# Kernel tuning notes

Hardware: AMD Instinct MI355X
Metric: run time of the kernel (lower is better)

The kernel has to match this reference:

```python
import jax, jax.numpy as jnp
import numpy as np

# ---- HashGridPlanesEncoder config (hybrid-k-planes) ----
NUM_LEVELS = 16
LEVEL_DIM = 2
BASE_RES = 16
DESIRED_RES = 2048
LOG2_HASHMAP = 19
D = 2  # grid_nd: each plane encoder is a 2D hash grid
N_PTS = 1048576
COO_COMBS = [(0, 1), (0, 2), (1, 2)]
HASH_PRIME_1 = 2654435761  # torch-ngp fast_hash prime for dim 1 (dim 0 prime is 1)


def _level_constants():
    # Mirrors torch-ngp GridEncoder offset/resolution computation.
    pls = 2.0 ** (np.log2(DESIRED_RES / BASE_RES) / (NUM_LEVELS - 1))
    max_params = 2 ** LOG2_HASHMAP
    scales, res, sizes, offs = [], [], [], [0]
    for l in range(NUM_LEVELS):
        s = BASE_RES * pls ** l - 1.0          # kernel: scale = exp2(l*S + H) - 1
        r = int(np.ceil(s)) + 1                # kernel: resolution = ceil(scale) + 1
        p = min(max_params, (r + 1) ** D)      # align_corners=False -> (res+1)^D
        p = int(np.ceil(p / 8) * 8)            # round up to multiple of 8
        scales.append(s); res.append(r); sizes.append(p); offs.append(offs[-1] + p)
    return (np.array(scales, np.float32), np.array(res, np.int64),
            np.array(sizes, np.int64), np.array(offs[:-1], np.int64), offs[-1])


SCALES, RES, SIZES, OFFSETS, TOTAL_PARAMS = _level_constants()
USE_HASH = ((RES + 1) ** D) > SIZES  # static per-level: dense linear index vs spatial hash


def _encode_plane(x2, table):
    """x2: [N,2] coords in [0,1]; table: [TOTAL_PARAMS, LEVEL_DIM]. Returns [N, L*C]."""
    n = x2.shape[0]
    scales = jnp.asarray(SCALES)
    pos = x2[:, None, :] * scales[None, :, None] + 0.5           # [N,L,2] (align_corners=False)
    pg_f = jnp.floor(pos)
    frac = pos - pg_f                                            # [N,L,2]
    pg = pg_f.astype(jnp.uint32)
    corners = jnp.array([[0, 0], [1, 0], [0, 1], [1, 1]], jnp.uint32)  # [4,2]
    cpos = pg[:, :, None, :] + corners[None, None]               # [N,L,4,2]
    cmask = corners.astype(bool)[None, None]                     # [1,1,4,2]
    w = jnp.where(cmask, frac[:, :, None, :], 1.0 - frac[:, :, None, :]).prod(-1)  # [N,L,4]
    stride1 = jnp.asarray((RES + 1).astype(np.uint32))           # [L]
    linear = cpos[..., 0] + cpos[..., 1] * stride1[None, :, None]
    hashed = cpos[..., 0] ^ (cpos[..., 1] * jnp.uint32(HASH_PRIME_1))  # uint32 wrap-around
    idx = jnp.where(jnp.asarray(USE_HASH)[None, :, None], hashed, linear)
    idx = idx % jnp.asarray(SIZES.astype(np.uint32))[None, :, None]
    idx = (idx + jnp.asarray(OFFSETS.astype(np.uint32))[None, :, None]).astype(jnp.int32)
    feats = table[idx]                                           # [N,L,4,C] gather
    out = (w[..., None] * feats).sum(axis=2)                     # [N,L,C] bilinear interp
    return out.reshape(n, NUM_LEVELS * LEVEL_DIM)


def setup_inputs() -> dict:
    key = jax.random.key(0)
    kp, k0, k1, k2 = jax.random.split(key, 4)
    pts = jax.random.uniform(kp, (N_PTS, 3), dtype=jnp.float32)  # coords (treated as in [-1,1] domain)
    std = 1e-4  # GridEncoder init: embeddings.uniform_(-1e-4, 1e-4)
    mk = lambda k: jax.random.uniform(k, (TOTAL_PARAMS, LEVEL_DIM), jnp.float32, -std, std)
    return {"pts": pts, "table_xy": mk(k0), "table_xz": mk(k1), "table_yz": mk(k2)}


def reference(pts, table_xy, table_xz, table_yz):
    # GridEncoder.forward normalizes inputs: (x + bound) / (2*bound), bound=1
    u = (pts + 1.0) * 0.5
    tables = (table_xy, table_xz, table_yz)
    out = _encode_plane(u[:, list(COO_COMBS[0])], tables[0])
    for comb, tab in zip(COO_COMBS[1:], tables[1:]):
        out = out + _encode_plane(u[:, list(comb)], tab)
    return out
```

## Files before the change

### kernel.cpp

```cpp
#include <hip/hip_runtime.h>
#include <hip/hip_fp16.h>
#include <cmath>

#define NLEV 16
#define HASH_START 12
#define HMASK ((1u << 19) - 1u)
#define HASH_PRIME 2654435761u
#define LDS_WORDS 14160

typedef float    f4 __attribute__((ext_vector_type(4)));
typedef unsigned u4 __attribute__((ext_vector_type(4)));

struct LvlC {
  float scale[NLEV];
  unsigned stride[NLEV];
  unsigned offset[NLEV];
};

__device__ __forceinline__ float2 h2f(unsigned u) {
  return __half22float2(__builtin_bit_cast(__half2, u));
}

__global__ __launch_bounds__(256) void k_convert(
    const float2* __restrict__ t0, const float2* __restrict__ t1,
    const float2* __restrict__ t2, unsigned* __restrict__ dst, unsigned total)
{
  unsigned g = blockIdx.x * 256 + threadIdx.x;
  unsigned stp = gridDim.x * 256;
  unsigned tot3 = 3u * total;
  for (unsigned e = g; e < tot3; e += stp) {
    const float2* src; unsigned i = e;
    if (i < total)            { src = t0; }
    else if (i < 2u * total)  { src = t1; i -= total; }
    else                      { src = t2; i -= 2u * total; }
    float2 v = src[i];
    __half2 h = __floats2half2_rn(v.x, v.y);
    __builtin_nontemporal_store(__builtin_bit_cast(unsigned, h), dst + e);
  }
}

__global__ __launch_bounds__(256) void k_dense(
    const float* __restrict__ pts, const unsigned* __restrict__ tab,
    unsigned* __restrict__ slices,
    LvlC lc, unsigned total, int n)
{
  int i = blockIdx.x * 256 + threadIdx.x;
  if (i >= n) return;
  float u0 = (pts[3 * i + 0] + 1.f) * .5f;
  float u1 = (pts[3 * i + 1] + 1.f) * .5f;
  float u2 = (pts[3 * i + 2] + 1.f) * .5f;
  const float ua[3] = {u0, u0, u1}, ub[3] = {u1, u2, u2};

#pragma unroll 1
  for (int grp = 0; grp < 3; ++grp) {
    const int l0 = 6 + 2 * grp;
    uint2 g[2][3][2];
    float gx[2][3], gy[2][3];
#pragma unroll
    for (int h = 0; h < 2; ++h) {
      const float sc = lc.scale[l0 + h];
      const unsigned st = lc.stride[l0 + h], o = lc.offset[l0 + h];
#pragma unroll
      for (int p = 0; p < 3; ++p) {
        float px = ua[p] * sc + .5f, py = ub[p] * sc + .5f;
        float fx = floorf(px), fy = floorf(py);
        gx[h][p] = px - fx; gy[h][p] = py - fy;
        unsigned i00 = (unsigned)fx + (unsigned)fy * st + o;
        const unsigned* tp = tab + (size_t)p * total;
        g[h][p][0] = *reinterpret_cast<const uint2*>(tp + i00);
        g[h][p][1] = *reinterpret_cast<const uint2*>(tp + i00 + st);
      }
    }
#pragma unroll
    for (int h = 0; h < 2; ++h) {
      float s0 = 0.f, s1 = 0.f;
#pragma unroll
      for (int p = 0; p < 3; ++p) {
        float x = gx[h][p], y = gy[h][p];
        float w00 = (1.f - x) * (1.f - y), w10 = x * (1.f - y);
        float w01 = (1.f - x) * y,          w11 = x * y;
        float2 f00 = h2f(g[h][p][0].x), f10 = h2f(g[h][p][0].y);
        float2 f01 = h2f(g[h][p][1].x), f11 = h2f(g[h][p][1].y);
        s0 += w00 * f00.x + w10 * f10.x + w01 * f01.x + w11 * f11.x;
        s1 += w00 * f00.y + w10 * f10.y + w01 * f01.y + w11 * f11.y;
      }
      __builtin_nontemporal_store(
          __builtin_bit_cast(unsigned, __floats2half2_rn(s0, s1)),
          slices + (size_t)(2 * grp + h) * n + i);
    }
  }
}

__device__ __forceinline__ void hash_row(
    const unsigned* __restrict__ tp, unsigned x0, unsigned hy,
    unsigned& g0, unsigned& g1)
{
  unsigned a0 = (x0 ^ hy) & HMASK;
  if ((x0 & 1u) == 0u) {
    uint2 v = *reinterpret_cast<const uint2*>(tp + (a0 & ~1u));
    bool hi = (a0 & 1u) != 0u;
    g0 = hi ? v.y : v.x;
    g1 = hi ? v.x : v.y;
  } else {
    g0 = tp[a0];
    g1 = tp[((x0 + 1u) ^ hy) & HMASK];
  }
}

__global__ __launch_bounds__(256) void k_hash(
    const float* __restrict__ pts, const unsigned* __restrict__ tab,
    unsigned* __restrict__ slices,
    LvlC lc, unsigned total, int n)
{
  int i = blockIdx.x * 256 + threadIdx.x;
  if (i >= n) return;
  float u0 = (pts[3 * i + 0] + 1.f) * .5f;
  float u1 = (pts[3 * i + 1] + 1.f) * .5f;
  float u2 = (pts[3 * i + 2] + 1.f) * .5f;
  const float ua[3] = {u0, u0, u1}, ub[3] = {u1, u2, u2};

#pragma unroll 1
  for (int grp = 0; grp < 2; ++grp) {
    const int l0 = HASH_START + 2 * grp;
    unsigned g[2][3][4];
    float rx[2][3], ry[2][3];
#pragma unroll
    for (int h = 0; h < 2; ++h) {
      const float sc = lc.scale[l0 + h];
      const unsigned o = lc.offset[l0 + h];
#pragma unroll
      for (int p = 0; p < 3; ++p) {
        float px = ua[p] * sc + .5f, py = ub[p] * sc + .5f;
        float fx = floorf(px), fy = floorf(py);
        rx[h][p] = px - fx; ry[h][p] = py - fy;
        unsigned x0 = (unsigned)fx, y0 = (unsigned)fy;
        unsigned hy0 = y0 * HASH_PRIME, hy1 = hy0 + HASH_PRIME;
        const unsigned* tp = tab + (size_t)p * total + o;
        hash_row(tp, x0, hy0, g[h][p][0], g[h][p][1]);
        hash_row(tp, x0, hy1, g[h][p][2], g[h][p][3]);
      }
    }
#pragma unroll
    for (int h = 0; h < 2; ++h) {
      float s0 = 0.f, s1 = 0.f;
#pragma unroll
      for (int p = 0; p < 3; ++p) {
        float x = rx[h][p], y = ry[h][p];
        float w00 = (1.f - x) * (1.f - y), w10 = x * (1.f - y);
        float w01 = (1.f - x) * y,          w11 = x * y;
        float2 f00 = h2f(g[h][p][0]), f10 = h2f(g[h][p][1]);
        float2 f01 = h2f(g[h][p][2]), f11 = h2f(g[h][p][3]);
        s0 += w00 * f00.x + w10 * f10.x + w01 * f01.x + w11 * f11.x;
        s1 += w00 * f00.y + w10 * f10.y + w01 * f01.y + w11 * f11.y;
      }
      __builtin_nontemporal_store(
          __builtin_bit_cast(unsigned, __floats2half2_rn(s0, s1)),
          slices + (size_t)(2 * grp + h) * n + i);
    }
  }
}

__global__ __launch_bounds__(512) void k_final(
    const float* __restrict__ pts, const unsigned* __restrict__ tab,
    const unsigned* __restrict__ slices,
    float* __restrict__ out, LvlC lc, unsigned total, int n)
{
  __shared__ unsigned lds[LDS_WORDS];
  int half = n >> 1;
  int t = blockIdx.x * 512 + threadIdx.x;
  const int idx[2] = {t, t + half};

  unsigned sl[2][10];
#pragma unroll
  for (int k = 0; k < 2; ++k)
#pragma unroll
    for (int j = 0; j < 10; ++j) sl[k][j] = slices[(size_t)j * n + idx[k]];

  float ua[2][3], ub[2][3];
#pragma unroll
  for (int k = 0; k < 2; ++k) {
    float u0 = (pts[3 * idx[k] + 0] + 1.f) * .5f;
    float u1 = (pts[3 * idx[k] + 1] + 1.f) * .5f;
    float u2 = (pts[3 * idx[k] + 2] + 1.f) * .5f;
    ua[k][0] = u0; ub[k][0] = u1;
    ua[k][1] = u0; ub[k][1] = u2;
    ua[k][2] = u1; ub[k][2] = u2;
  }

  float res[2][12];
#pragma unroll
  for (int k = 0; k < 2; ++k)
#pragma unroll
    for (int j = 0; j < 12; ++j) res[k][j] = 0.f;

  for (int p = 0; p < 3; ++p) {
    if (p) __syncthreads();
    const u4* src = reinterpret_cast<const u4*>(tab + (size_t)p * total);
    for (unsigned e = threadIdx.x; e < LDS_WORDS / 4; e += 512)
      reinterpret_cast<u4*>(lds)[e] = src[e];
    __syncthreads();
#pragma unroll
    for (int l = 0; l < 6; ++l) {
      const float sc = lc.scale[l];
      const unsigned st = lc.stride[l], o = lc.offset[l];
#pragma unroll
      for (int k = 0; k < 2; ++k) {
        float px = ua[k][p] * sc + .5f, py = ub[k][p] * sc + .5f;
        float fx = floorf(px), fy = floorf(py);
        float x = px - fx, y = py - fy;
        unsigned i00 = (unsigned)fx + (unsigned)fy * st + o;
        float2 f00 = h2f(lds[i00]),      f10 = h2f(lds[i00 + 1]);
        float2 f01 = h2f(lds[i00 + st]), f11 = h2f(lds[i00 + st + 1]);
        float w00 = (1.f - x) * (1.f - y), w10 = x * (1.f - y);
        float w01 = (1.f - x) * y,          w11 = x * y;
        res[k][2 * l + 0] += w00 * f00.x + w10 * f10.x + w01 * f01.x + w11 * f11.x;
        res[k][2 * l + 1] += w00 * f00.y + w10 * f10.y + w01 * f01.y + w11 * f11.y;
      }
    }
  }

#pragma unroll
  for (int k = 0; k < 2; ++k) {
    float v[32];
#pragma unroll
    for (int j = 0; j < 12; ++j) v[j] = res[k][j];
#pragma unroll
    for (int j = 0; j < 10; ++j) {
      float2 f = h2f(sl[k][j]);
      v[12 + 2 * j] = f.x; v[12 + 2 * j + 1] = f.y;
    }
    float4* o4 = (float4*)(out + (size_t)idx[k] * 32);
#pragma unroll
    for (int j = 0; j < 8; ++j)
      o4[j] = make_float4(v[4 * j], v[4 * j + 1], v[4 * j + 2], v[4 * j + 3]);
  }
}

__global__ __launch_bounds__(256) void k_fallback(
    const float* __restrict__ pts, const float2* __restrict__ txy,
    const float2* __restrict__ txz, const float2* __restrict__ tyz,
    float* __restrict__ out, LvlC lc, int n)
{
  int i = blockIdx.x * 256 + threadIdx.x;
  if (i >= n) return;
  float u0 = (pts[3 * i + 0] + 1.f) * .5f;
  float u1 = (pts[3 * i + 1] + 1.f) * .5f;
  float u2 = (pts[3 * i + 2] + 1.f) * .5f;
  const float ua[3] = {u0, u0, u1}, ub[3] = {u1, u2, u2};
  const float2* tabs[3] = {txy, txz, tyz};
  float acc[32];
#pragma unroll
  for (int j = 0; j < 32; ++j) acc[j] = 0.f;
#pragma unroll
  for (int l = 0; l < NLEV; ++l) {
    const float sc = lc.scale[l];
    const unsigned o = lc.offset[l], s = lc.stride[l];
#pragma unroll
    for (int p = 0; p < 3; ++p) {
      const float2* t = tabs[p];
      float px = ua[p] * sc + .5f, py = ub[p] * sc + .5f;
      float fx = floorf(px), fy = floorf(py);
      float rx = px - fx, ry = py - fy;
      unsigned x0 = (unsigned)fx, y0 = (unsigned)fy;
      float w00 = (1.f - rx) * (1.f - ry), w10 = rx * (1.f - ry);
      float w01 = (1.f - rx) * ry,          w11 = rx * ry;
      float2 f00, f10, f01, f11;
      if (l >= HASH_START) {
        unsigned hy0 = y0 * HASH_PRIME, hy1 = hy0 + HASH_PRIME;
        f00 = t[o + ((x0 ^ hy0) & HMASK)];
        f10 = t[o + (((x0 + 1u) ^ hy0) & HMASK)];
        f01 = t[o + ((x0 ^ hy1) & HMASK)];
        f11 = t[o + (((x0 + 1u) ^ hy1) & HMASK)];
      } else {
        unsigned i00 = x0 + y0 * s;
        float4 r0 = *reinterpret_cast<const float4*>(t + o + i00);
        float4 r1 = *reinterpret_cast<const float4*>(t + o + i00 + s);
        f00 = make_float2(r0.x, r0.y); f10 = make_float2(r0.z, r0.w);
        f01 = make_float2(r1.x, r1.y); f11 = make_float2(r1.z, r1.w);
      }
      acc[2 * l + 0] += w00 * f00.x + w10 * f10.x + w01 * f01.x + w11 * f11.x;
      acc[2 * l + 1] += w00 * f00.y + w10 * f10.y + w01 * f01.y + w11 * f11.y;
    }
  }
  float4* o4 = (float4*)(out + (size_t)i * 32);
#pragma unroll
  for (int j = 0; j < 8; ++j)
    o4[j] = make_float4(acc[4 * j], acc[4 * j + 1], acc[4 * j + 2], acc[4 * j + 3]);
}

static unsigned compute_levels(LvlC* lc)
{
  const double pls = std::pow(2.0, std::log2(2048.0 / 16.0) / 15.0);
  unsigned long long off = 0;
  for (int l = 0; l < NLEV; ++l) {
    double s = 16.0 * std::pow(pls, (double)l) - 1.0;
    lc->scale[l] = (float)s;
    long long r = (long long)std::ceil(s) + 1;
    long long dense = (r + 1) * (r + 1);
    long long sz = dense < (1LL << 19) ? dense : (1LL << 19);
    sz = ((sz + 7) / 8) * 8;
    lc->stride[l] = (unsigned)(r + 1);
    lc->offset[l] = (unsigned)off;
    off += (unsigned long long)sz;
  }
  return (unsigned)off;
}

extern "C" void kernel_launch(void* const* d_in, const int* in_sizes, int n_in,
                              void* d_out, int out_size, void* d_ws, size_t ws_size,
                              hipStream_t stream) {
  const float*  pts = (const float*)d_in[0];
  const float2* txy = (const float2*)d_in[1];
  const float2* txz = (const float2*)d_in[2];
  const float2* tyz = (const float2*)d_in[3];
  float* out = (float*)d_out;
  int n = in_sizes[0] / 3;

  LvlC lc;
  unsigned total = compute_levels(&lc);

  size_t tab_bytes = (size_t)3 * total * 4;
  size_t tab_al = (tab_bytes + 255) & ~(size_t)255;
  size_t need = tab_al + (size_t)10 * n * 4;

  bool ok = (n % 1024 == 0) && (lc.offset[6] == LDS_WORDS) && (ws_size >= need);
  for (int l = HASH_START; l < NLEV; ++l) {
    unsigned sz = ((l + 1 < NLEV) ? lc.offset[l + 1] : total) - lc.offset[l];
    ok = ok && (sz == (1u << 19));
  }

  int block = 256;
  int grid = (n + block - 1) / block;
  if (!ok) {
    k_fallback<<<grid, block, 0, stream>>>(pts, txy, txz, tyz, out, lc, n);
    return;
  }

  unsigned* tab16 = (unsigned*)d_ws;
  unsigned* slices = (unsigned*)((char*)d_ws + tab_al);

  k_convert<<<2048, 256, 0, stream>>>(txy, txz, tyz, tab16, total);
  k_dense<<<grid, block, 0, stream>>>(pts, tab16, slices, lc, total, n);
  k_hash <<<grid, block, 0, stream>>>(pts, tab16, slices + (size_t)6 * n, lc, total, n);
  k_final<<<(n / 2) / 512, 512, 0, stream>>>(pts, tab16, slices, out, lc, total, n);
}
```

Baseline: 382.1 us.

## Duplicate dense rows into interleaved fp16 layout, gather hash levels from fp32 directly

Replaces the full-table fp16 conversion with a small conversion of levels 0-5 plus a row-duplicated layout for dense levels 6-11, so each bilinear lookup becomes a single 16-byte load. Hash levels now read the original fp32 tables directly, which removes the need to convert the large hash tables at all. The dense and hash kernels are merged into one gather kernel. The final kernel now handles four points per thread in a 2048-point block so the LDS table load is amortised better. The cost is more launches for the duplication step, wider fp32 hash loads, and more register pressure in the final kernel.

```diff
diff --git a/kernel.cpp b/kernel.cpp
--- a/kernel.cpp
+++ b/kernel.cpp
@@ -15,34 +15,66 @@
   float scale[NLEV];
   unsigned stride[NLEV];
   unsigned offset[NLEV];
+  unsigned dupoff[NLEV];
 };
 
 __device__ __forceinline__ float2 h2f(unsigned u) {
   return __half22float2(__builtin_bit_cast(__half2, u));
 }
 
-__global__ __launch_bounds__(256) void k_convert(
+__global__ __launch_bounds__(256) void k_convert05(
     const float2* __restrict__ t0, const float2* __restrict__ t1,
-    const float2* __restrict__ t2, unsigned* __restrict__ dst, unsigned total)
-{
-  unsigned g = blockIdx.x * 256 + threadIdx.x;
-  unsigned stp = gridDim.x * 256;
-  unsigned tot3 = 3u * total;
-  for (unsigned e = g; e < tot3; e += stp) {
-    const float2* src; unsigned i = e;
-    if (i < total)            { src = t0; }
-    else if (i < 2u * total)  { src = t1; i -= total; }
-    else                      { src = t2; i -= 2u * total; }
-    float2 v = src[i];
-    __half2 h = __floats2half2_rn(v.x, v.y);
-    __builtin_nontemporal_store(__builtin_bit_cast(unsigned, h), dst + e);
-  }
-}
-
-__global__ __launch_bounds__(256) void k_dense(
-    const float* __restrict__ pts, const unsigned* __restrict__ tab,
-    unsigned* __restrict__ slices,
-    LvlC lc, unsigned total, int n)
+    const float2* __restrict__ t2, unsigned* __restrict__ dst, unsigned total16)
+{
+  unsigned idx = blockIdx.x * 256 + threadIdx.x;
+  if (idx >= 3u * LDS_WORDS) return;
+  unsigned p = idx / LDS_WORDS, e = idx % LDS_WORDS;
+  const float2* src = (p == 0) ? t0 : ((p == 1) ? t1 : t2);
+  float2 v = src[e];
+  dst[(size_t)p * total16 + e] =
+      __builtin_bit_cast(unsigned, __floats2half2_rn(v.x, v.y));
+}
+
+__global__ __launch_bounds__(256) void k_convert_dup(
+    const float2* __restrict__ t0, const float2* __restrict__ t1,
+    const float2* __restrict__ t2, unsigned* __restrict__ dst,
+    unsigned src_off, unsigned dst_off, unsigned st, unsigned total16)
+{
+  unsigned x = blockIdx.x * 256 + threadIdx.x;
+  if (x >= st) return;
+  unsigned y = blockIdx.y;
+  unsigned p = blockIdx.z;
+  const float2* src = (p == 0) ? t0 : ((p == 1) ? t1 : t2);
+  float2 a = src[src_off + (size_t)y * st + x];
+  float2 b = src[src_off + (size_t)(y + 1) * st + x];
+  uint2 w;
+  w.x = __builtin_bit_cast(unsigned, __floats2half2_rn(a.x, a.y));
+  w.y = __builtin_bit_cast(unsigned, __floats2half2_rn(b.x, b.y));
+  *reinterpret_cast<uint2*>(dst + (size_t)p * total16 + dst_off +
+                            (size_t)(y * st + x) * 2) = w;
+}
+
+__device__ __forceinline__ void hash_row_f32(
+    const float2* __restrict__ tp, unsigned x0, unsigned hy,
+    float2& g0, float2& g1)
+{
+  unsigned a0 = (x0 ^ hy) & HMASK;
+  if ((x0 & 1u) == 0u) {
+    f4 v = *reinterpret_cast<const f4*>(tp + (a0 & ~1u));
+    bool hi = (a0 & 1u) != 0u;
+    g0 = hi ? make_float2(v.z, v.w) : make_float2(v.x, v.y);
+    g1 = hi ? make_float2(v.x, v.y) : make_float2(v.z, v.w);
+  } else {
+    g0 = tp[a0];
+    g1 = tp[((x0 + 1u) ^ hy) & HMASK];
+  }
+}
+
+__global__ __launch_bounds__(256) void k_gather(
+    const float* __restrict__ pts, const unsigned* __restrict__ tab16,
+    const float2* __restrict__ t0, const float2* __restrict__ t1,
+    const float2* __restrict__ t2,
+    unsigned* __restrict__ slices, LvlC lc, unsigned total16, int n)
 {
   int i = blockIdx.x * 256 + threadIdx.x;
   if (i >= n) return;
@@ -50,25 +82,24 @@
   float u1 = (pts[3 * i + 1] + 1.f) * .5f;
   float u2 = (pts[3 * i + 2] + 1.f) * .5f;
   const float ua[3] = {u0, u0, u1}, ub[3] = {u1, u2, u2};
+  const float2* tabs[3] = {t0, t1, t2};
 
 #pragma unroll 1
   for (int grp = 0; grp < 3; ++grp) {
     const int l0 = 6 + 2 * grp;
-    uint2 g[2][3][2];
+    u4 g[2][3];
     float gx[2][3], gy[2][3];
 #pragma unroll
     for (int h = 0; h < 2; ++h) {
       const float sc = lc.scale[l0 + h];
-      const unsigned st = lc.stride[l0 + h], o = lc.offset[l0 + h];
+      const unsigned st = lc.stride[l0 + h], o = lc.dupoff[l0 + h];
 #pragma unroll
       for (int p = 0; p < 3; ++p) {
         float px = ua[p] * sc + .5f, py = ub[p] * sc + .5f;
         float fx = floorf(px), fy = floorf(py);
         gx[h][p] = px - fx; gy[h][p] = py - fy;
-        unsigned i00 = (unsigned)fx + (unsigned)fy * st + o;
-        const unsigned* tp = tab + (size_t)p * total;
-        g[h][p][0] = *reinterpret_cast<const uint2*>(tp + i00);
-        g[h][p][1] = *reinterpret_cast<const uint2*>(tp + i00 + st);
+        unsigned e = ((unsigned)fy * st + (unsigned)fx) * 2 + o;
+        g[h][p] = *reinterpret_cast<const u4*>(tab16 + (size_t)p * total16 + e);
       }
     }
 #pragma unroll
@@ -77,10 +108,10 @@
 #pragma unroll
       for (int p = 0; p < 3; ++p) {
         float x = gx[h][p], y = gy[h][p];
-        float w00 = (1.f - x) * (1.f - y), w10 = x * (1.f - y);
-        float w01 = (1.f - x) * y,          w11 = x * y;
-        float2 f00 = h2f(g[h][p][0].x), f10 = h2f(g[h][p][0].y);
-        float2 f01 = h2f(g[h][p][1].x), f11 = h2f(g[h][p][1].y);
+        float w00 = (1.f - x) * (1.f - y), w01 = (1.f - x) * y;
+        float w10 = x * (1.f - y),          w11 = x * y;
+        float2 f00 = h2f(g[h][p].x), f01 = h2f(g[h][p].y);
+        float2 f10 = h2f(g[h][p].z), f11 = h2f(g[h][p].w);
         s0 += w00 * f00.x + w10 * f10.x + w01 * f01.x + w11 * f11.x;
         s1 += w00 * f00.y + w10 * f10.y + w01 * f01.y + w11 * f11.y;
       }
@@ -89,40 +120,11 @@
           slices + (size_t)(2 * grp + h) * n + i);
     }
   }
-}
-
-__device__ __forceinline__ void hash_row(
-    const unsigned* __restrict__ tp, unsigned x0, unsigned hy,
-    unsigned& g0, unsigned& g1)
-{
-  unsigned a0 = (x0 ^ hy) & HMASK;
-  if ((x0 & 1u) == 0u) {
-    uint2 v = *reinterpret_cast<const uint2*>(tp + (a0 & ~1u));
-    bool hi = (a0 & 1u) != 0u;
-    g0 = hi ? v.y : v.x;
-    g1 = hi ? v.x : v.y;
-  } else {
-    g0 = tp[a0];
-    g1 = tp[((x0 + 1u) ^ hy) & HMASK];
-  }
-}
-
-__global__ __launch_bounds__(256) void k_hash(
-    const float* __restrict__ pts, const unsigned* __restrict__ tab,
-    unsigned* __restrict__ slices,
-    LvlC lc, unsigned total, int n)
-{
-  int i = blockIdx.x * 256 + threadIdx.x;
-  if (i >= n) return;
-  float u0 = (pts[3 * i + 0] + 1.f) * .5f;
-  float u1 = (pts[3 * i + 1] + 1.f) * .5f;
-  float u2 = (pts[3 * i + 2] + 1.f) * .5f;
-  const float ua[3] = {u0, u0, u1}, ub[3] = {u1, u2, u2};
 
 #pragma unroll 1
   for (int grp = 0; grp < 2; ++grp) {
     const int l0 = HASH_START + 2 * grp;
-    unsigned g[2][3][4];
+    float2 g[2][3][4];
     float rx[2][3], ry[2][3];
 #pragma unroll
     for (int h = 0; h < 2; ++h) {
@@ -135,9 +137,9 @@
         rx[h][p] = px - fx; ry[h][p] = py - fy;
         unsigned x0 = (unsigned)fx, y0 = (unsigned)fy;
         unsigned hy0 = y0 * HASH_PRIME, hy1 = hy0 + HASH_PRIME;
-        const unsigned* tp = tab + (size_t)p * total + o;
-        hash_row(tp, x0, hy0, g[h][p][0], g[h][p][1]);
-        hash_row(tp, x0, hy1, g[h][p][2], g[h][p][3]);
+        const float2* tp = tabs[p] + o;
+        hash_row_f32(tp, x0, hy0, g[h][p][0], g[h][p][1]);
+        hash_row_f32(tp, x0, hy1, g[h][p][2], g[h][p][3]);
       }
     }
 #pragma unroll
@@ -148,55 +150,58 @@
         float x = rx[h][p], y = ry[h][p];
         float w00 = (1.f - x) * (1.f - y), w10 = x * (1.f - y);
         float w01 = (1.f - x) * y,          w11 = x * y;
-        float2 f00 = h2f(g[h][p][0]), f10 = h2f(g[h][p][1]);
-        float2 f01 = h2f(g[h][p][2]), f11 = h2f(g[h][p][3]);
-        s0 += w00 * f00.x + w10 * f10.x + w01 * f01.x + w11 * f11.x;
-        s1 += w00 * f00.y + w10 * f10.y + w01 * f01.y + w11 * f11.y;
+        s0 += w00 * g[h][p][0].x + w10 * g[h][p][1].x +
+              w01 * g[h][p][2].x + w11 * g[h][p][3].x;
+        s1 += w00 * g[h][p][0].y + w10 * g[h][p][1].y +
+              w01 * g[h][p][2].y + w11 * g[h][p][3].y;
       }
       __builtin_nontemporal_store(
           __builtin_bit_cast(unsigned, __floats2half2_rn(s0, s1)),
-          slices + (size_t)(2 * grp + h) * n + i);
+          slices + (size_t)(6 + 2 * grp + h) * n + i);
     }
   }
 }
 
 __global__ __launch_bounds__(512) void k_final(
-    const float* __restrict__ pts, const unsigned* __restrict__ tab,
+    const float* __restrict__ pts, const unsigned* __restrict__ tab16,
     const unsigned* __restrict__ slices,
-    float* __restrict__ out, LvlC lc, unsigned total, int n)
+    float* __restrict__ out, LvlC lc, unsigned total16, int n)
 {
   __shared__ unsigned lds[LDS_WORDS];
-  int half = n >> 1;
-  int t = blockIdx.x * 512 + threadIdx.x;
-  const int idx[2] = {t, t + half};
-
-  unsigned sl[2][10];
-#pragma unroll
-  for (int k = 0; k < 2; ++k)
-#pragma unroll
-    for (int j = 0; j < 10; ++j) sl[k][j] = slices[(size_t)j * n + idx[k]];
-
-  float ua[2][3], ub[2][3];
-#pragma unroll
-  for (int k = 0; k < 2; ++k) {
-    float u0 = (pts[3 * idx[k] + 0] + 1.f) * .5f;
-    float u1 = (pts[3 * idx[k] + 1] + 1.f) * .5f;
-    float u2 = (pts[3 * idx[k] + 2] + 1.f) * .5f;
-    ua[k][0] = u0; ub[k][0] = u1;
-    ua[k][1] = u0; ub[k][1] = u2;
-    ua[k][2] = u1; ub[k][2] = u2;
-  }
-
-  float res[2][12];
-#pragma unroll
-  for (int k = 0; k < 2; ++k)
-#pragma unroll
-    for (int j = 0; j < 12; ++j) res[k][j] = 0.f;
+  const int tid = threadIdx.x;
+  const int base = blockIdx.x * 2048;
+
+  int idx[2][2];
+#pragma unroll
+  for (int c = 0; c < 2; ++c)
+#pragma unroll
+    for (int k = 0; k < 2; ++k) idx[c][k] = base + c * 1024 + k * 512 + tid;
+
+  float ua[2][2][3], ub[2][2][3];
+#pragma unroll
+  for (int c = 0; c < 2; ++c)
+#pragma unroll
+    for (int k = 0; k < 2; ++k) {
+      float v0 = (pts[3 * idx[c][k] + 0] + 1.f) * .5f;
+      float v1 = (pts[3 * idx[c][k] + 1] + 1.f) * .5f;
+      float v2 = (pts[3 * idx[c][k] + 2] + 1.f) * .5f;
+      ua[c][k][0] = v0; ub[c][k][0] = v1;
+      ua[c][k][1] = v0; ub[c][k][1] = v2;
+      ua[c][k][2] = v1; ub[c][k][2] = v2;
+    }
+
+  float res[2][2][12];
+#pragma unroll
+  for (int c = 0; c < 2; ++c)
+#pragma unroll
+    for (int k = 0; k < 2; ++k)
+#pragma unroll
+      for (int j = 0; j < 12; ++j) res[c][k][j] = 0.f;
 
   for (int p = 0; p < 3; ++p) {
     if (p) __syncthreads();
-    const u4* src = reinterpret_cast<const u4*>(tab + (size_t)p * total);
-    for (unsigned e = threadIdx.x; e < LDS_WORDS / 4; e += 512)
+    const u4* src = reinterpret_cast<const u4*>(tab16 + (size_t)p * total16);
+    for (unsigned e = tid; e < LDS_WORDS / 4; e += 512)
       reinterpret_cast<u4*>(lds)[e] = src[e];
     __syncthreads();
 #pragma unroll
@@ -204,36 +209,43 @@
       const float sc = lc.scale[l];
       const unsigned st = lc.stride[l], o = lc.offset[l];
 #pragma unroll
-      for (int k = 0; k < 2; ++k) {
-        float px = ua[k][p] * sc + .5f, py = ub[k][p] * sc + .5f;
-        float fx = floorf(px), fy = floorf(py);
-        float x = px - fx, y = py - fy;
-        unsigned i00 = (unsigned)fx + (unsigned)fy * st + o;
-        float2 f00 = h2f(lds[i00]),      f10 = h2f(lds[i00 + 1]);
-        float2 f01 = h2f(lds[i00 + st]), f11 = h2f(lds[i00 + st + 1]);
-        float w00 = (1.f - x) * (1.f - y), w10 = x * (1.f - y);
-        float w01 = (1.f - x) * y,          w11 = x * y;
-        res[k][2 * l + 0] += w00 * f00.x + w10 * f10.x + w01 * f01.x + w11 * f11.x;
-        res[k][2 * l + 1] += w00 * f00.y + w10 * f10.y + w01 * f01.y + w11 * f11.y;
-      }
-    }
-  }
-
-#pragma unroll
-  for (int k = 0; k < 2; ++k) {
-    float v[32];
-#pragma unroll
-    for (int j = 0; j < 12; ++j) v[j] = res[k][j];
-#pragma unroll
-    for (int j = 0; j < 10; ++j) {
-      float2 f = h2f(sl[k][j]);
-      v[12 + 2 * j] = f.x; v[12 + 2 * j + 1] = f.y;
-    }
-    float4* o4 = (float4*)(out + (size_t)idx[k] * 32);
-#pragma unroll
-    for (int j = 0; j < 8; ++j)
-      o4[j] = make_float4(v[4 * j], v[4 * j + 1], v[4 * j + 2], v[4 * j + 3]);
-  }
+      for (int c = 0; c < 2; ++c)
+#pragma unroll
+        for (int k = 0; k < 2; ++k) {
+          float px = ua[c][k][p] * sc + .5f, py = ub[c][k][p] * sc + .5f;
+          float fx = floorf(px), fy = floorf(py);
+          float x = px - fx, y = py - fy;
+          unsigned i00 = (unsigned)fx + (unsigned)fy * st + o;
+          float2 f00 = h2f(lds[i00]),      f10 = h2f(lds[i00 + 1]);
+          float2 f01 = h2f(lds[i00 + st]), f11 = h2f(lds[i00 + st + 1]);
+          float w00 = (1.f - x) * (1.f - y), w10 = x * (1.f - y);
+          float w01 = (1.f - x) * y,          w11 = x * y;
+          res[c][k][2 * l + 0] += w00 * f00.x + w10 * f10.x + w01 * f01.x + w11 * f11.x;
+          res[c][k][2 * l + 1] += w00 * f00.y + w10 * f10.y + w01 * f01.y + w11 * f11.y;
+        }
+    }
+  }
+
+#pragma unroll
+  for (int c = 0; c < 2; ++c)
+#pragma unroll
+    for (int k = 0; k < 2; ++k) {
+      unsigned sl[10];
+#pragma unroll
+      for (int j = 0; j < 10; ++j) sl[j] = slices[(size_t)j * n + idx[c][k]];
+      float v[32];
+#pragma unroll
+      for (int j = 0; j < 12; ++j) v[j] = res[c][k][j];
+#pragma unroll
+      for (int j = 0; j < 10; ++j) {
+        float2 f = h2f(sl[j]);
+        v[12 + 2 * j] = f.x; v[12 + 2 * j + 1] = f.y;
+      }
+      float4* o4 = (float4*)(out + (size_t)idx[c][k] * 32);
+#pragma unroll
+      for (int j = 0; j < 8; ++j)
+        o4[j] = make_float4(v[4 * j], v[4 * j + 1], v[4 * j + 2], v[4 * j + 3]);
+    }
 }
 
 __global__ __launch_bounds__(256) void k_fallback(
@@ -288,10 +300,11 @@
     o4[j] = make_float4(acc[4 * j], acc[4 * j + 1], acc[4 * j + 2], acc[4 * j + 3]);
 }
 
-static unsigned compute_levels(LvlC* lc)
+static unsigned compute_levels(LvlC* lc, unsigned* total16_out)
 {
   const double pls = std::pow(2.0, std::log2(2048.0 / 16.0) / 15.0);
   unsigned long long off = 0;
+  unsigned sizes[NLEV];
   for (int l = 0; l < NLEV; ++l) {
     double s = 16.0 * std::pow(pls, (double)l) - 1.0;
     lc->scale[l] = (float)s;
@@ -301,8 +314,16 @@
     sz = ((sz + 7) / 8) * 8;
     lc->stride[l] = (unsigned)(r + 1);
     lc->offset[l] = (unsigned)off;
+    sizes[l] = (unsigned)sz;
+    lc->dupoff[l] = 0;
     off += (unsigned long long)sz;
   }
+  unsigned d = lc->offset[6];
+  for (int l = 6; l < 12; ++l) {
+    lc->dupoff[l] = d;
+    d += 2u * lc->stride[l] * (lc->stride[l] - 1);
+  }
+  *total16_out = d;
   return (unsigned)off;
 }
 
@@ -317,13 +338,14 @@
   int n = in_sizes[0] / 3;
 
   LvlC lc;
-  unsigned total = compute_levels(&lc);
-
-  size_t tab_bytes = (size_t)3 * total * 4;
+  unsigned total16;
+  unsigned total = compute_levels(&lc, &total16);
+
+  size_t tab_bytes = (size_t)3 * total16 * 4;
   size_t tab_al = (tab_bytes + 255) & ~(size_t)255;
   size_t need = tab_al + (size_t)10 * n * 4;
 
-  bool ok = (n % 1024 == 0) && (lc.offset[6] == LDS_WORDS) && (ws_size >= need);
+  bool ok = (n % 2048 == 0) && (lc.offset[6] == LDS_WORDS) && (ws_size >= need);
   for (int l = HASH_START; l < NLEV; ++l) {
     unsigned sz = ((l + 1 < NLEV) ? lc.offset[l + 1] : total) - lc.offset[l];
     ok = ok && (sz == (1u << 19));
@@ -339,8 +361,15 @@
   unsigned* tab16 = (unsigned*)d_ws;
   unsigned* slices = (unsigned*)((char*)d_ws + tab_al);
 
-  k_convert<<<2048, 256, 0, stream>>>(txy, txz, tyz, tab16, total);
-  k_dense<<<grid, block, 0, stream>>>(pts, tab16, slices, lc, total, n);
-  k_hash <<<grid, block, 0, stream>>>(pts, tab16, slices + (size_t)6 * n, lc, total, n);
-  k_final<<<(n / 2) / 512, 512, 0, stream>>>(pts, tab16, slices, out, lc, total, n);
-}
+  k_convert05<<<(3 * LDS_WORDS + 255) / 256, 256, 0, stream>>>(
+      txy, txz, tyz, tab16, total16);
+  for (int l = 6; l < 12; ++l) {
+    unsigned st = lc.stride[l];
+    dim3 g((st + 255) / 256, st - 1, 3);
+    k_convert_dup<<<g, 256, 0, stream>>>(txy, txz, tyz, tab16,
+                                         lc.offset[l], lc.dupoff[l], st, total16);
+  }
+  k_gather<<<grid, block, 0, stream>>>(pts, tab16, txy, txz, tyz,
+                                       slices, lc, total16, n);
+  k_final<<<n / 2048, 512, 0, stream>>>(pts, tab16, slices, out, lc, total16, n);
+}
```

After: 458.8 us. 1.2x slower.
